# Performance work log

Measured on AMD Instinct MI355X. Metric: run time of the kernel, lower is better.

Reference implementation:

```python
import jax, jax.numpy as jnp
import numpy as np

N = 50000      # nodes
E = 800000     # edges (before self-loops)
F_IN = 256     # feature_size
H = 96         # hidden_channels
G = 64         # graphs in batch
NC = 4         # num_classes
EPS = 1e-5     # BatchNorm eps


def _lrelu(x, s=0.01):
    return jnp.where(x >= 0, x, s * x)


def _gat(x, W, a_s, a_d, b, src, dst):
    # PyG GATConv, heads=1: linear transform, edge-wise LeakyReLU(0.2) scores,
    # segment softmax over destination nodes, scatter-add aggregation.
    h = x @ W                                                  # [N,H]
    e = _lrelu((h * a_s).sum(-1)[src] + (h * a_d).sum(-1)[dst], 0.2)  # [E+N]
    m = jax.ops.segment_max(e, dst, num_segments=N)
    ee = jnp.exp(e - m[dst])
    denom = jax.ops.segment_sum(ee, dst, num_segments=N)
    alpha = ee / denom[dst]
    return jax.ops.segment_sum(alpha[:, None] * h[src], dst, num_segments=N) + b


def _bn(x, g, b):
    # training-mode BatchNorm over the node dimension
    mu = x.mean(0)
    var = ((x - mu) ** 2).mean(0)
    return g * (x - mu) / jnp.sqrt(var + EPS) + b


def setup_inputs() -> dict:
    key = jax.random.key(0)
    ks = jax.random.split(key, 20)
    p = lambda i, sh: jax.random.normal(ks[i], sh, jnp.float32) * 0.05
    inp = {
        "x": jax.random.normal(ks[0], (N, F_IN), jnp.float32),
        "edge_index": jax.random.randint(ks[1], (2, E), 0, N),
        "batch": jnp.sort(jax.random.randint(ks[2], (N,), 0, G)),
        "embed_W": p(3, (F_IN, H)), "embed_b": jnp.zeros((H,), jnp.float32),
        "conv1_W": p(4, (H, H)), "conv1_as": p(5, (H,)), "conv1_ad": p(6, (H,)), "conv1_b": jnp.zeros((H,), jnp.float32),
        "conv2_W": p(7, (H, H)), "conv2_as": p(8, (H,)), "conv2_ad": p(9, (H,)), "conv2_b": jnp.zeros((H,), jnp.float32),
        "conv3_W": p(10, (H, H)), "conv3_as": p(11, (H,)), "conv3_ad": p(12, (H,)), "conv3_b": jnp.zeros((H,), jnp.float32),
        "fc1_W": p(13, (H, H)), "fc1_b": jnp.zeros((H,), jnp.float32),
        "fc2_W": p(14, (H, H)), "fc2_b": jnp.zeros((H,), jnp.float32),
        "bn1_g": jnp.ones((H,), jnp.float32), "bn1_b": jnp.zeros((H,), jnp.float32),
        "bn2_g": jnp.ones((H,), jnp.float32), "bn2_b": jnp.zeros((H,), jnp.float32),
        "bn3_g": jnp.ones((H,), jnp.float32), "bn3_b": jnp.zeros((H,), jnp.float32),
        "fc3_W": p(15, (H, H // 2)), "fc3_b": jnp.zeros((H // 2,), jnp.float32),
        "fc4_W": p(16, (H // 2, NC)), "fc4_b": jnp.zeros((NC,), jnp.float32),
    }
    return inp


def reference(x, edge_index, batch, embed_W, embed_b,
              conv1_W, conv1_as, conv1_ad, conv1_b,
              conv2_W, conv2_as, conv2_ad, conv2_b,
              conv3_W, conv3_as, conv3_ad, conv3_b,
              fc1_W, fc1_b, fc2_W, fc2_b,
              bn1_g, bn1_b, bn2_g, bn2_b, bn3_g, bn3_b,
              fc3_W, fc3_b, fc4_W, fc4_b):
    loops = jnp.arange(N)
    src = jnp.concatenate([edge_index[0], loops])   # GATConv add_self_loops=True
    dst = jnp.concatenate([edge_index[1], loops])

    h = _lrelu(x @ embed_W + embed_b)
    identity = h
    h = _lrelu(_bn(_gat(h, conv1_W, conv1_as, conv1_ad, conv1_b, src, dst), bn1_g, bn1_b)) + identity
    h = _lrelu(h @ fc1_W + fc1_b)
    h = _lrelu(_bn(_gat(h, conv2_W, conv2_as, conv2_ad, conv2_b, src, dst), bn2_g, bn2_b)) + identity
    h = _lrelu(h @ fc2_W + fc2_b)
    h = _lrelu(_bn(_gat(h, conv3_W, conv3_as, conv3_ad, conv3_b, src, dst), bn3_g, bn3_b)) + identity

    # Poincare ball expmap0 with c=1: tanh(||u||) * u / ||u||
    n = jnp.maximum(jnp.linalg.norm(h, axis=-1, keepdims=True), 1e-15)
    h = jnp.tanh(n) * h / n

    cnt = jax.ops.segment_sum(jnp.ones((N,), h.dtype), batch, num_segments=G)
    pooled = jax.ops.segment_sum(h, batch, num_segments=G) / jnp.maximum(cnt, 1.0)[:, None]

    o = _lrelu(pooled @ fc3_W + fc3_b)
    return o @ fc4_W + fc4_b
```

## Files before the change

kernel.cpp:

```cpp
#include <hip/hip_runtime.h>
#include <hip/hip_bf16.h>

#define DEVINL __device__ __forceinline__

constexpr int N_NODES = 50000;
constexpr int N_EDGES = 800000;
constexpr int F_IN    = 256;
constexpr int H       = 96;
constexpr int NG      = 64;
constexpr float BN_EPS = 1e-5f;
constexpr int SLOT    = 64;
constexpr int NREP    = 8;
constexpr int REPSZ   = NG * H + NG;
constexpr int EPB     = 8;
constexpr int ECHUNK  = 256 * EPB;

typedef short bf16x8 __attribute__((ext_vector_type(8)));
typedef float f32x4  __attribute__((ext_vector_type(4)));

DEVINL float bf2f(unsigned int u) {
    union { unsigned int i; float f; } c; c.i = u << 16; return c.f;
}
DEVINL unsigned short f2bf(float f) {
    union { float f; unsigned int i; } c; c.f = f;
    unsigned int x = c.i;
    return (unsigned short)((x + 0x7fffu + ((x >> 16) & 1u)) >> 16);
}
DEVINL float lrelu01(float v) { return v >= 0.f ? v : 0.01f * v; }
DEVINL float ldf(const void* p, size_t i, int f32) {
    return f32 ? ((const float*)p)[i] : bf2f(((const unsigned short*)p)[i]);
}

__global__ __launch_bounds__(256) void detect_fill_k(const unsigned short* __restrict__ x,
                                                     int* __restrict__ flag,
                                                     int* __restrict__ fill)
{
    if (blockIdx.x == 0 && threadIdx.x < 64) {
        int l = threadIdx.x;
        float f = bf2f(x[l]);
        bool huge = !(fabsf(f) <= 1e4f);
        unsigned long long m = __ballot(huge);
        if (l == 0) flag[0] = (__popcll(m) >= 8) ? 1 : 0;
    }
    int i = blockIdx.x * 256 + threadIdx.x;
    if (i < N_NODES) fill[i] = 0;
}

__global__ __launch_bounds__(256) void wpackall_k(
    const void* __restrict__ sE, const void* __restrict__ s0,
    const void* __restrict__ s1, const void* __restrict__ s2,
    const void* __restrict__ s3, const void* __restrict__ s4,
    const int* __restrict__ dflag,
    unsigned short* __restrict__ dE, unsigned short* __restrict__ d0,
    unsigned short* __restrict__ d1, unsigned short* __restrict__ d2,
    unsigned short* __restrict__ d3, unsigned short* __restrict__ d4)
{
    int b = blockIdx.x;
    const void* src; unsigned short* dst; int K, i0;
    if (b < 96) { src = sE; dst = dE; K = F_IN; i0 = b * 256; }
    else {
        int m = (b - 96) / 36, r = (b - 96) % 36;
        K = H; i0 = r * 256;
        if      (m == 0) { src = s0; dst = d0; }
        else if (m == 1) { src = s1; dst = d1; }
        else if (m == 2) { src = s2; dst = d2; }
        else if (m == 3) { src = s3; dst = d3; }
        else             { src = s4; dst = d4; }
    }
    int i = i0 + threadIdx.x;
    if (i >= K * 96) return;
    int c   = i / 3072;
    int rem = i - c * 3072;
    int t    = rem >> 9;
    int rem2 = rem & 511;
    int l = rem2 >> 3, j = rem2 & 7;
    int k = c * 32 + (l >> 4) * 8 + j;
    int n = t * 16 + (l & 15);
    if (dflag[0]) dst[i] = f2bf(((const float*)src)[k * 96 + n]);
    else          dst[i] = ((const unsigned short*)src)[k * 96 + n];
}

template<int EPI, int AWS, int SD, int ABN, int SCAT, int K>
__global__ __launch_bounds__(256, 4) void mgemm_k(
    const void* __restrict__ Ap, const unsigned short* __restrict__ Wpk,
    const void* __restrict__ bp, const int* __restrict__ dflag,
    unsigned short* __restrict__ out, unsigned short* __restrict__ out2,
    const void* __restrict__ as_, const void* __restrict__ ad_,
    float* __restrict__ s, float* __restrict__ d,
    const float* __restrict__ coefp, const unsigned short* __restrict__ idn,
    const int* __restrict__ ei, int* __restrict__ fill,
    unsigned short* __restrict__ colw, int e0, int e1, int nscat,
    int M)
{
    constexpr int NCH = K / 32;

    if (SCAT && (int)blockIdx.x < nscat) {
        int b0 = e0 + (int)blockIdx.x * ECHUNK + (int)threadIdx.x;
        int sv[EPB], dv[EPB];
        bool ok[EPB];
        #pragma unroll
        for (int j = 0; j < EPB; j++) {
            int e = b0 + j * 256;
            ok[j] = (e < e1);
            int ee = ok[j] ? e : e0;
            sv[j] = ei[ee];
            dv[j] = ei[N_EDGES + ee];
        }
        int p[EPB];
        #pragma unroll
        for (int j = 0; j < EPB; j++)
            p[j] = ok[j] ? atomicAdd(&fill[dv[j]], 1) : SLOT;
        #pragma unroll
        for (int j = 0; j < EPB; j++)
            if (p[j] < SLOT) colw[(size_t)dv[j] * SLOT + p[j]] = (unsigned short)sv[j];
        return;
    }

    const int gb   = SCAT ? (int)blockIdx.x - nscat : (int)blockIdx.x;
    const int f32  = AWS ? 0 : dflag[0];
    const int wf32 = dflag[0];
    const int l    = threadIdx.x & 63;
    const int wave = threadIdx.x >> 6;
    const int row0 = gb * 64 + wave * 16;
    const int m    = l & 15;
    const int q    = l >> 4;
    const int arow = row0 + m;
    const bool aok = arow < M;

    bf16x8 av[NCH];
    #pragma unroll
    for (int c = 0; c < NCH; c++) {
        bf16x8 a = {};
        if (aok) {
            if (ABN) {
                const int f0 = c * 32 + q * 8;
                uint4 xu = *(const uint4*)((const unsigned short*)Ap + (size_t)arow * K + f0);
                uint4 iu = *(const uint4*)(idn + (size_t)arow * K + f0);
                unsigned int xs[4] = { xu.x, xu.y, xu.z, xu.w };
                unsigned int is[4] = { iu.x, iu.y, iu.z, iu.w };
                #pragma unroll
                for (int jj = 0; jj < 4; jj++) {
                    int f = f0 + 2 * jj;
                    float v0 = lrelu01(bf2f(xs[jj] & 0xffff) * coefp[f]     + coefp[96 + f])     + bf2f(is[jj] & 0xffff);
                    float v1 = lrelu01(bf2f(xs[jj] >> 16)    * coefp[f + 1] + coefp[96 + f + 1]) + bf2f(is[jj] >> 16);
                    a[2 * jj]     = (short)f2bf(v0);
                    a[2 * jj + 1] = (short)f2bf(v1);
                }
            } else if (f32) {
                const float* A = (const float*)Ap + (size_t)arow * K + c * 32 + q * 8;
                #pragma unroll
                for (int j = 0; j < 8; j++) a[j] = (short)f2bf(A[j]);
            } else {
                a = *(const bf16x8*)((const unsigned short*)Ap + (size_t)arow * K + c * 32 + q * 8);
            }
        }
        av[c] = a;
    }

    f32x4 acc[6] = {};
    const bf16x8* wp = (const bf16x8*)Wpk;
    #pragma unroll
    for (int c = 0; c < NCH; c++) {
        const int base = c * 384 + l;
        #pragma unroll
        for (int t = 0; t < 6; t++)
            acc[t] = __builtin_amdgcn_mfma_f32_16x16x32_bf16(av[c], wp[base + t * 64], acc[t], 0, 0, 0);
    }

    float bv[6];
    if (EPI > 0) {
        #pragma unroll
        for (int t = 0; t < 6; t++) bv[t] = ldf(bp, t * 16 + m, wf32);
    }
    #pragma unroll
    for (int r = 0; r < 4; r++) {
        int rr = row0 + q * 4 + r;
        if (rr >= M) continue;
        size_t o = (size_t)rr * 96 + m;
        #pragma unroll
        for (int t = 0; t < 6; t++) {
            float v = acc[t][r];
            if (EPI > 0) v = lrelu01(v + bv[t]);
            unsigned short sv = f2bf(v);
            out[o + t * 16] = sv;
            if (EPI == 2) out2[o + t * 16] = sv;
        }
    }

    if (SD) {
        float asv[6], adv[6];
        #pragma unroll
        for (int t = 0; t < 6; t++) {
            asv[t] = ldf(as_, t * 16 + m, wf32);
            adv[t] = ldf(ad_, t * 16 + m, wf32);
        }
        #pragma unroll
        for (int r = 0; r < 4; r++) {
            float ps = 0.f, pd = 0.f;
            #pragma unroll
            for (int t = 0; t < 6; t++) {
                ps = fmaf(acc[t][r], asv[t], ps);
                pd = fmaf(acc[t][r], adv[t], pd);
            }
            #pragma unroll
            for (int off = 1; off < 16; off <<= 1) {
                ps += __shfl_xor(ps, off);
                pd += __shfl_xor(pd, off);
            }
            int rr = row0 + q * 4 + r;
            if (m == 0 && rr < M) { s[rr] = ps; d[rr] = pd; }
        }
    }
}

__global__ __launch_bounds__(256) void agg_k(
    const unsigned short* __restrict__ h2, const float* __restrict__ s,
    const float* __restrict__ d, const int* __restrict__ fill,
    const unsigned short* __restrict__ col, const void* __restrict__ bias,
    const int* __restrict__ dflag, unsigned short* __restrict__ out,
    float* __restrict__ bnsum, float* __restrict__ zp, int M)
{
    __shared__ uint2 uwb[4][80];
    if (blockIdx.x == 0 && threadIdx.x < 192) bnsum[threadIdx.x] = 0.f;
    if (zp) {
        int zi = blockIdx.x * 256 + threadIdx.x;
        if (zi < NREP * REPSZ) zp[zi] = 0.f;
    }
    int f32 = dflag[0];
    int v = (blockIdx.x * blockDim.x + threadIdx.x) >> 6;
    int l = threadIdx.x & 63;
    int wv = threadIdx.x >> 6;
    if (v >= M) return;
    int st   = v * SLOT;
    int degr = min(fill[v], SLOT - 1);
    int deg  = degr + 1;

    float dv = d[v];
    int u = 0; float e = -1e30f;
    if (l < degr) {
        u = col[st + l];
        float t = s[u] + dv;
        e = t >= 0.f ? t : 0.2f * t;
    } else if (l == degr) {
        u = v;
        float t = s[v] + dv;
        e = t >= 0.f ? t : 0.2f * t;
    }
    float lm = e;
    #pragma unroll
    for (int off = 32; off > 0; off >>= 1) lm = fmaxf(lm, __shfl_xor(lm, off));
    float w = (l < deg) ? __expf(e - lm) : 0.f;
    float ls = w;
    #pragma unroll
    for (int off = 32; off > 0; off >>= 1) ls += __shfl_xor(ls, off);
    float rden = 1.0f / ls;

    uwb[wv][l] = make_uint2((unsigned int)u, __float_as_uint(w));
    if (l < 16) uwb[wv][64 + l] = make_uint2(0u, 0u);

    bool hw = (l < 48);
    int  c2 = 2 * l;
    float a0 = 0.f, a1 = 0.f;
    const uint2* myuw = uwb[wv];
    for (int j = 0; j < deg; j += 16) {
        uint2 p[16];
        #pragma unroll
        for (int k = 0; k < 16; k++) p[k] = myuw[j + k];
        if (hw) {
            unsigned int hv[16];
            #pragma unroll
            for (int k = 0; k < 16; k++)
                hv[k] = *(const unsigned int*)(h2 + (size_t)p[k].x * 96 + c2);
            #pragma unroll
            for (int k = 0; k < 16; k++) {
                float wj = __uint_as_float(p[k].y);
                a0 = fmaf(wj, bf2f(hv[k] & 0xffff), a0);
                a1 = fmaf(wj, bf2f(hv[k] >> 16),    a1);
            }
        }
    }
    if (hw) {
        float b0 = ldf(bias, c2,     f32);
        float b1 = ldf(bias, c2 + 1, f32);
        unsigned int o = (unsigned int)f2bf(a0 * rden + b0)
                       | ((unsigned int)f2bf(a1 * rden + b1) << 16);
        *(unsigned int*)(out + (size_t)v * 96 + c2) = o;
    }
}

__global__ __launch_bounds__(192) void bnstats_k(const unsigned short* __restrict__ x,
                                                 float* __restrict__ sums, int M)
{
    int c  = threadIdx.x % 96;
    int g2 = threadIdx.x / 96;
    float s = 0.f, q = 0.f;
    for (int r = blockIdx.x * 2 + g2; r < M; r += gridDim.x * 2) {
        float v = bf2f(x[(size_t)r * 96 + c]);
        s += v; q += v * v;
    }
    __shared__ float lsd[192], lqd[192];
    lsd[threadIdx.x] = s; lqd[threadIdx.x] = q;
    __syncthreads();
    if (g2 == 0) {
        atomicAdd(&sums[c],      s + lsd[threadIdx.x + 96]);
        atomicAdd(&sums[96 + c], q + lqd[threadIdx.x + 96]);
    }
}

__global__ void bncoef_k(const float* __restrict__ sums,
                         const void* __restrict__ g_,
                         const void* __restrict__ b_,
                         const int* __restrict__ dflag,
                         float* __restrict__ coef)
{
    int c = threadIdx.x;
    if (c >= 96) return;
    int f32 = dflag[0];
    float mu  = sums[c] * (1.f / N_NODES);
    float var = sums[96 + c] * (1.f / N_NODES) - mu * mu;
    float rinv = 1.0f / sqrtf(var + BN_EPS);
    float sc = ldf(g_, c, f32) * rinv;
    coef[c]      = sc;
    coef[96 + c] = ldf(b_, c, f32) - mu * sc;
}

__global__ __launch_bounds__(256) void bnpool_k(
    const unsigned short* __restrict__ h, const float* __restrict__ coef,
    const unsigned short* __restrict__ iden, const int* __restrict__ batch,
    float* __restrict__ pooled8, int M)
{
    int w = (blockIdx.x * blockDim.x + threadIdx.x) >> 6;
    int l = threadIdx.x & 63;
    int v0 = w * 16;
    if (v0 >= M) return;
    float* P = pooled8 + (blockIdx.x & (NREP - 1)) * REPSZ;
    float* C = P + NG * H;
    bool hw = (l < 48);
    int  c2 = 2 * l;
    float sc0 = 0.f, sc1 = 0.f, sh0 = 0.f, sh1 = 0.f;
    if (hw) {
        sc0 = coef[c2]; sc1 = coef[c2 + 1];
        sh0 = coef[96 + c2]; sh1 = coef[97 + c2];
    }
    int nv = min(16, M - v0);

    int gb[16];
    #pragma unroll
    for (int k = 0; k < 16; k++) gb[k] = batch[v0 + min(k, nv - 1)];

    float x0[16], x1[16], q[16];
    #pragma unroll
    for (int k = 0; k < 16; k++) { x0[k] = 0.f; x1[k] = 0.f; q[k] = 0.f; }
    if (hw) {
        unsigned int xu[16], iu[16];
        #pragma unroll
        for (int k = 0; k < 16; k++) {
            int v = v0 + k;
            if (k < nv) {
                xu[k] = *(const unsigned int*)(h    + (size_t)v * 96 + c2);
                iu[k] = *(const unsigned int*)(iden + (size_t)v * 96 + c2);
            } else { xu[k] = 0u; iu[k] = 0u; }
        }
        #pragma unroll
        for (int k = 0; k < 16; k++) {
            x0[k] = lrelu01(bf2f(xu[k] & 0xffff) * sc0 + sh0) + bf2f(iu[k] & 0xffff);
            x1[k] = lrelu01(bf2f(xu[k] >> 16)    * sc1 + sh1) + bf2f(iu[k] >> 16);
            q[k]  = x0[k] * x0[k] + x1[k] * x1[k];
        }
    }

    #pragma unroll
    for (int off = 32; off > 0; off >>= 1) {
        #pragma unroll
        for (int k = 0; k < 16; k++) q[k] += __shfl_xor(q[k], off);
    }

    float f[16];
    #pragma unroll
    for (int k = 0; k < 16; k++) {
        float n = fmaxf(sqrtf(q[k]), 1e-15f);
        if (n < 15.f) {
            float t = __expf(2.f * n);
            f[k] = (t - 1.f) / ((t + 1.f) * n);
        } else {
            f[k] = 1.f / n;
        }
    }

    float a0 = 0.f, a1 = 0.f, cnt = 0.f;
    int curg = -1;
    for (int k = 0; k < nv; k++) {
        int g = gb[k];
        if (g != curg) {
            if (curg >= 0) {
                if (hw) {
                    atomicAdd(&P[curg * 96 + c2],     a0);
                    atomicAdd(&P[curg * 96 + c2 + 1], a1);
                }
                if (l == 0) atomicAdd(&C[curg], cnt);
            }
            a0 = a1 = 0.f; cnt = 0.f; curg = g;
        }
        a0 = fmaf(f[k], x0[k], a0);
        a1 = fmaf(f[k], x1[k], a1);
        cnt += 1.f;
    }
    if (curg >= 0) {
        if (hw) {
            atomicAdd(&P[curg * 96 + c2],     a0);
            atomicAdd(&P[curg * 96 + c2 + 1], a1);
        }
        if (l == 0) atomicAdd(&C[curg], cnt);
    }
}

__global__ __launch_bounds__(64) void head_k(const float* __restrict__ pooled8,
                                             const void* __restrict__ w3,
                                             const void* __restrict__ b3,
                                             const void* __restrict__ w4,
                                             const void* __restrict__ b4,
                                             const int* __restrict__ dflag,
                                             void* __restrict__ outv)
{
    int g = blockIdx.x;
    int t = threadIdx.x;
    int f32 = dflag[0];
    __shared__ float p[96];
    __shared__ float o[48];
    float cs = 0.f;
    #pragma unroll
    for (int r = 0; r < NREP; r++) cs += pooled8[r * REPSZ + NG * H + g];
    float inv = 1.0f / fmaxf(cs, 1.0f);
    for (int c = t; c < 96; c += 64) {
        float v = 0.f;
        #pragma unroll
        for (int r = 0; r < NREP; r++) v += pooled8[r * REPSZ + g * 96 + c];
        p[c] = v * inv;
    }
    __syncthreads();
    if (t < 48) {
        float a = ldf(b3, t, f32);
        #pragma unroll
        for (int c = 0; c < 96; c++) a = fmaf(p[c], ldf(w3, (size_t)c * 48 + t, f32), a);
        o[t] = lrelu01(a);
    }
    __syncthreads();
    if (t < 4) {
        float a = ldf(b4, t, f32);
        #pragma unroll
        for (int j = 0; j < 48; j++) a = fmaf(o[j], ldf(w4, j * 4 + t, f32), a);
        if (f32) ((float*)outv)[g * 4 + t] = a;
        else     ((unsigned short*)outv)[g * 4 + t] = f2bf(a);
    }
}

extern "C" void kernel_launch(void* const* d_in, const int* in_sizes, int n_in,
                              void* d_out, int out_size, void* d_ws, size_t ws_size,
                              hipStream_t stream)
{
    const void* x     = d_in[0];
    const int*  ei    = (const int*)d_in[1];
    const int*  batch = (const int*)d_in[2];
    const void* embW  = d_in[3];
    const void* embB  = d_in[4];
    const void* convW[3]  = { d_in[5],  d_in[9],  d_in[13] };
    const void* convAs[3] = { d_in[6],  d_in[10], d_in[14] };
    const void* convAd[3] = { d_in[7],  d_in[11], d_in[15] };
    const void* convB[3]  = { d_in[8],  d_in[12], d_in[16] };
    const void* fcW[2]    = { d_in[17], d_in[19] };
    const void* fcB[2]    = { d_in[18], d_in[20] };
    const void* bnG[3]    = { d_in[21], d_in[23], d_in[25] };
    const void* bnB[3]    = { d_in[22], d_in[24], d_in[26] };
    const void* fc3W = d_in[27];
    const void* fc3b = d_in[28];
    const void* fc4W = d_in[29];
    const void* fc4b = d_in[30];

    char* wp_ = (char*)d_ws;
    auto alloc = [&](size_t b) { char* p = wp_; wp_ += (b + 255) & ~(size_t)255; return p; };
    int*   dflag = (int*)alloc(256);
    unsigned short* ident = (unsigned short*)alloc((size_t)N_NODES * H * 2);
    unsigned short* hA    = (unsigned short*)alloc((size_t)N_NODES * H * 2);
    unsigned short* hB    = (unsigned short*)alloc((size_t)N_NODES * H * 2);
    float* s_sc  = (float*)alloc((size_t)N_NODES * 4);
    float* d_sc  = (float*)alloc((size_t)N_NODES * 4);
    float* bnsum = (float*)alloc(192 * 4);
    float* coef  = (float*)alloc(192 * 4);
    float* pooled8 = (float*)alloc((size_t)NREP * REPSZ * 4);
    int*   fill  = (int*)alloc((size_t)N_NODES * 4);
    unsigned short* col = (unsigned short*)alloc((size_t)N_NODES * SLOT * 2);
    unsigned short* wpkEmb = (unsigned short*)alloc((size_t)F_IN * 96 * 2);
    unsigned short* wpkS[5];
    for (int i = 0; i < 5; i++) wpkS[i] = (unsigned short*)alloc((size_t)H * 96 * 2);

    const int GM = (N_NODES + 63) / 64;
    const int GW = (N_NODES * 64 + 255) / 256;
    const int GP = ((N_NODES + 15) / 16 * 64 + 255) / 256;
    const int GF = (N_NODES + 255) / 256;
    const int EH = N_EDGES / 2;
    const int GS = (EH + ECHUNK - 1) / ECHUNK;

    detect_fill_k<<<GF, 256, 0, stream>>>((const unsigned short*)x, dflag, fill);

    wpackall_k<<<276, 256, 0, stream>>>(embW, convW[0], convW[1], convW[2], fcW[0], fcW[1],
                                        dflag, wpkEmb, wpkS[0], wpkS[1], wpkS[2], wpkS[3], wpkS[4]);

    mgemm_k<1, 0, 0, 0, 1, F_IN><<<GS + GM, 256, 0, stream>>>(
        x, wpkEmb, embB, dflag, ident, nullptr,
        nullptr, nullptr, nullptr, nullptr, nullptr, nullptr,
        ei, fill, col, 0, EH, GS, N_NODES);

    unsigned short* hcur = hA;
    unsigned short* htmp = hB;

    for (int l = 0; l < 3; l++) {
        if (l == 0) {
            mgemm_k<0, 1, 1, 0, 1, H><<<GS + GM, 256, 0, stream>>>(
                ident, wpkS[0], nullptr, dflag, htmp, nullptr,
                convAs[0], convAd[0], s_sc, d_sc, nullptr, nullptr,
                ei, fill, col, EH, N_EDGES, GS, N_NODES);
        } else {
            mgemm_k<0, 1, 1, 0, 0, H><<<GM, 256, 0, stream>>>(
                hcur, wpkS[l], nullptr, dflag, htmp, nullptr,
                convAs[l], convAd[l], s_sc, d_sc, nullptr, nullptr,
                nullptr, nullptr, nullptr, 0, 0, 0, N_NODES);
        }
        agg_k<<<GW, 256, 0, stream>>>(htmp, s_sc, d_sc, fill, col, convB[l], dflag, hcur,
                                      bnsum, (l == 2) ? pooled8 : nullptr, N_NODES);
        bnstats_k<<<512, 192, 0, stream>>>(hcur, bnsum, N_NODES);
        bncoef_k<<<1, 128, 0, stream>>>(bnsum, bnG[l], bnB[l], dflag, coef);
        if (l < 2) {
            mgemm_k<1, 1, 0, 1, 0, H><<<GM, 256, 0, stream>>>(
                hcur, wpkS[3 + l], fcB[l], dflag, htmp, nullptr,
                nullptr, nullptr, nullptr, nullptr, coef, ident,
                nullptr, nullptr, nullptr, 0, 0, 0, N_NODES);
            unsigned short* t = hcur; hcur = htmp; htmp = t;
        }
    }

    bnpool_k<<<GP, 256, 0, stream>>>(hcur, coef, ident, batch, pooled8, N_NODES);
    head_k<<<NG, 64, 0, stream>>>(pooled8, fc3W, fc3b, fc4W, fc4b, dflag, d_out);
}
```

Baseline: 437.5 us.

## Fuse BN stats into aggregation, fuse fc and conv GEMMs, merge setup kernels

BatchNorm sum and sum-of-squares are now computed inside the aggregation kernel from the values it just wrote. Each block reduces them in shared memory and adds atomically into 64 replicated accumulators, which replaces the separate bnstats pass that re-read the whole feature matrix. The BN-apply, fc GEMM and next conv GEMM are fused into one kernel that passes the intermediate tile through shared memory, and the detect/fill and weight-pack kernels are merged into one. This removes several launches and full-array round trips, at the cost of more atomics and a longer serial reduction in bncoef.

```diff
diff --git a/kernel.cpp b/kernel.cpp
--- a/kernel.cpp
+++ b/kernel.cpp
@@ -14,6 +14,8 @@
 constexpr int REPSZ   = NG * H + NG;
 constexpr int EPB     = 8;
 constexpr int ECHUNK  = 256 * EPB;
+constexpr int BNREP   = 64;
+constexpr int GFILL   = (N_NODES + 255) / 256;
 
 typedef short bf16x8 __attribute__((ext_vector_type(8)));
 typedef float f32x4  __attribute__((ext_vector_type(4)));
@@ -31,35 +33,39 @@
     return f32 ? ((const float*)p)[i] : bf2f(((const unsigned short*)p)[i]);
 }
 
-__global__ __launch_bounds__(256) void detect_fill_k(const unsigned short* __restrict__ x,
-                                                     int* __restrict__ flag,
-                                                     int* __restrict__ fill)
-{
-    if (blockIdx.x == 0 && threadIdx.x < 64) {
-        int l = threadIdx.x;
-        float f = bf2f(x[l]);
-        bool huge = !(fabsf(f) <= 1e4f);
-        unsigned long long m = __ballot(huge);
-        if (l == 0) flag[0] = (__popcll(m) >= 8) ? 1 : 0;
-    }
-    int i = blockIdx.x * 256 + threadIdx.x;
-    if (i < N_NODES) fill[i] = 0;
-}
-
-__global__ __launch_bounds__(256) void wpackall_k(
+__global__ __launch_bounds__(256) void setup_k(
+    const unsigned short* __restrict__ x,
+    int* __restrict__ flag, int* __restrict__ fill,
     const void* __restrict__ sE, const void* __restrict__ s0,
     const void* __restrict__ s1, const void* __restrict__ s2,
     const void* __restrict__ s3, const void* __restrict__ s4,
-    const int* __restrict__ dflag,
     unsigned short* __restrict__ dE, unsigned short* __restrict__ d0,
     unsigned short* __restrict__ d1, unsigned short* __restrict__ d2,
     unsigned short* __restrict__ d3, unsigned short* __restrict__ d4)
 {
     int b = blockIdx.x;
+    if (b < GFILL) {
+        if (b == 0 && threadIdx.x < 64) {
+            int l = threadIdx.x;
+            float f = bf2f(x[l]);
+            bool huge = !(fabsf(f) <= 1e4f);
+            unsigned long long m = __ballot(huge);
+            if (l == 0) flag[0] = (__popcll(m) >= 8) ? 1 : 0;
+        }
+        int i = b * 256 + threadIdx.x;
+        if (i < N_NODES) fill[i] = 0;
+        return;
+    }
+    float ff = bf2f(x[threadIdx.x & 63]);
+    bool huge = !(fabsf(ff) <= 1e4f);
+    unsigned long long mm = __ballot(huge);
+    int lf32 = (__popcll(mm) >= 8) ? 1 : 0;
+
+    int bb = b - GFILL;
     const void* src; unsigned short* dst; int K, i0;
-    if (b < 96) { src = sE; dst = dE; K = F_IN; i0 = b * 256; }
+    if (bb < 96) { src = sE; dst = dE; K = F_IN; i0 = bb * 256; }
     else {
-        int m = (b - 96) / 36, r = (b - 96) % 36;
+        int m = (bb - 96) / 36, r = (bb - 96) % 36;
         K = H; i0 = r * 256;
         if      (m == 0) { src = s0; dst = d0; }
         else if (m == 1) { src = s1; dst = d1; }
@@ -76,11 +82,11 @@
     int l = rem2 >> 3, j = rem2 & 7;
     int k = c * 32 + (l >> 4) * 8 + j;
     int n = t * 16 + (l & 15);
-    if (dflag[0]) dst[i] = f2bf(((const float*)src)[k * 96 + n]);
-    else          dst[i] = ((const unsigned short*)src)[k * 96 + n];
-}
-
-template<int EPI, int AWS, int SD, int ABN, int SCAT, int K>
+    if (lf32) dst[i] = f2bf(((const float*)src)[k * 96 + n]);
+    else      dst[i] = ((const unsigned short*)src)[k * 96 + n];
+}
+
+template<int EPI, int AWS, int SD, int ABN, int SCAT, int K, int ZB>
 __global__ __launch_bounds__(256, 4) void mgemm_k(
     const void* __restrict__ Ap, const unsigned short* __restrict__ Wpk,
     const void* __restrict__ bp, const int* __restrict__ dflag,
@@ -90,9 +96,14 @@
     const float* __restrict__ coefp, const unsigned short* __restrict__ idn,
     const int* __restrict__ ei, int* __restrict__ fill,
     unsigned short* __restrict__ colw, int e0, int e1, int nscat,
-    int M)
+    float* __restrict__ bnsumR, int M)
 {
     constexpr int NCH = K / 32;
+
+    if (ZB) {
+        int zi = blockIdx.x * 256 + threadIdx.x;
+        if (zi < BNREP * 192) bnsumR[zi] = 0.f;
+    }
 
     if (SCAT && (int)blockIdx.x < nscat) {
         int b0 = e0 + (int)blockIdx.x * ECHUNK + (int)threadIdx.x;
@@ -213,15 +224,135 @@
     }
 }
 
+__global__ __launch_bounds__(256, 4) void fcconv_k(
+    const unsigned short* __restrict__ Ap,
+    const unsigned short* __restrict__ Wfc, const void* __restrict__ bfc,
+    const unsigned short* __restrict__ Wcv,
+    const int* __restrict__ dflag,
+    unsigned short* __restrict__ out,
+    const void* __restrict__ as_, const void* __restrict__ ad_,
+    float* __restrict__ s, float* __restrict__ d,
+    const float* __restrict__ coefp, const unsigned short* __restrict__ idn,
+    float* __restrict__ bnsumR, int M)
+{
+    __shared__ unsigned short R[64][104];
+
+    {
+        int zi = blockIdx.x * 256 + threadIdx.x;
+        if (zi < BNREP * 192) bnsumR[zi] = 0.f;
+    }
+
+    const int wf32 = dflag[0];
+    const int l    = threadIdx.x & 63;
+    const int wave = threadIdx.x >> 6;
+    const int row0 = blockIdx.x * 64 + wave * 16;
+    const int m    = l & 15;
+    const int q    = l >> 4;
+    const int arow = row0 + m;
+    const bool aok = arow < M;
+
+    bf16x8 av[3];
+    #pragma unroll
+    for (int c = 0; c < 3; c++) {
+        bf16x8 a = {};
+        if (aok) {
+            const int f0 = c * 32 + q * 8;
+            uint4 xu = *(const uint4*)(Ap  + (size_t)arow * H + f0);
+            uint4 iu = *(const uint4*)(idn + (size_t)arow * H + f0);
+            unsigned int xs[4] = { xu.x, xu.y, xu.z, xu.w };
+            unsigned int is[4] = { iu.x, iu.y, iu.z, iu.w };
+            #pragma unroll
+            for (int jj = 0; jj < 4; jj++) {
+                int f = f0 + 2 * jj;
+                float v0 = lrelu01(bf2f(xs[jj] & 0xffff) * coefp[f]     + coefp[96 + f])     + bf2f(is[jj] & 0xffff);
+                float v1 = lrelu01(bf2f(xs[jj] >> 16)    * coefp[f + 1] + coefp[96 + f + 1]) + bf2f(is[jj] >> 16);
+                a[2 * jj]     = (short)f2bf(v0);
+                a[2 * jj + 1] = (short)f2bf(v1);
+            }
+        }
+        av[c] = a;
+    }
+
+    f32x4 acc[6] = {};
+    const bf16x8* wp1 = (const bf16x8*)Wfc;
+    #pragma unroll
+    for (int c = 0; c < 3; c++) {
+        const int base = c * 384 + l;
+        #pragma unroll
+        for (int t = 0; t < 6; t++)
+            acc[t] = __builtin_amdgcn_mfma_f32_16x16x32_bf16(av[c], wp1[base + t * 64], acc[t], 0, 0, 0);
+    }
+
+    float bv[6];
+    #pragma unroll
+    for (int t = 0; t < 6; t++) bv[t] = ldf(bfc, t * 16 + m, wf32);
+    #pragma unroll
+    for (int r = 0; r < 4; r++) {
+        int lr = wave * 16 + q * 4 + r;
+        #pragma unroll
+        for (int t = 0; t < 6; t++)
+            R[lr][t * 16 + m] = f2bf(lrelu01(acc[t][r] + bv[t]));
+    }
+    __syncthreads();
+
+    bf16x8 a2[3];
+    #pragma unroll
+    for (int c = 0; c < 3; c++)
+        a2[c] = *(const bf16x8*)&R[wave * 16 + m][c * 32 + q * 8];
+
+    f32x4 acc2[6] = {};
+    const bf16x8* wp2 = (const bf16x8*)Wcv;
+    #pragma unroll
+    for (int c = 0; c < 3; c++) {
+        const int base = c * 384 + l;
+        #pragma unroll
+        for (int t = 0; t < 6; t++)
+            acc2[t] = __builtin_amdgcn_mfma_f32_16x16x32_bf16(a2[c], wp2[base + t * 64], acc2[t], 0, 0, 0);
+    }
+
+    #pragma unroll
+    for (int r = 0; r < 4; r++) {
+        int rr = row0 + q * 4 + r;
+        if (rr >= M) continue;
+        size_t o = (size_t)rr * 96 + m;
+        #pragma unroll
+        for (int t = 0; t < 6; t++)
+            out[o + t * 16] = f2bf(acc2[t][r]);
+    }
+
+    float asv[6], adv[6];
+    #pragma unroll
+    for (int t = 0; t < 6; t++) {
+        asv[t] = ldf(as_, t * 16 + m, wf32);
+        adv[t] = ldf(ad_, t * 16 + m, wf32);
+    }
+    #pragma unroll
+    for (int r = 0; r < 4; r++) {
+        float ps = 0.f, pd = 0.f;
+        #pragma unroll
+        for (int t = 0; t < 6; t++) {
+            ps = fmaf(acc2[t][r], asv[t], ps);
+            pd = fmaf(acc2[t][r], adv[t], pd);
+        }
+        #pragma unroll
+        for (int off = 1; off < 16; off <<= 1) {
+            ps += __shfl_xor(ps, off);
+            pd += __shfl_xor(pd, off);
+        }
+        int rr = row0 + q * 4 + r;
+        if (m == 0 && rr < M) { s[rr] = ps; d[rr] = pd; }
+    }
+}
+
 __global__ __launch_bounds__(256) void agg_k(
     const unsigned short* __restrict__ h2, const float* __restrict__ s,
     const float* __restrict__ d, const int* __restrict__ fill,
     const unsigned short* __restrict__ col, const void* __restrict__ bias,
     const int* __restrict__ dflag, unsigned short* __restrict__ out,
-    float* __restrict__ bnsum, float* __restrict__ zp, int M)
+    float* __restrict__ bnsumR, float* __restrict__ zp, int M)
 {
     __shared__ uint2 uwb[4][80];
-    if (blockIdx.x == 0 && threadIdx.x < 192) bnsum[threadIdx.x] = 0.f;
+    __shared__ float lstat[4][192];
     if (zp) {
         int zi = blockIdx.x * 256 + threadIdx.x;
         if (zi < NREP * REPSZ) zp[zi] = 0.f;
@@ -230,98 +361,107 @@
     int v = (blockIdx.x * blockDim.x + threadIdx.x) >> 6;
     int l = threadIdx.x & 63;
     int wv = threadIdx.x >> 6;
-    if (v >= M) return;
-    int st   = v * SLOT;
-    int degr = min(fill[v], SLOT - 1);
-    int deg  = degr + 1;
-
-    float dv = d[v];
-    int u = 0; float e = -1e30f;
-    if (l < degr) {
-        u = col[st + l];
-        float t = s[u] + dv;
-        e = t >= 0.f ? t : 0.2f * t;
-    } else if (l == degr) {
-        u = v;
-        float t = s[v] + dv;
-        e = t >= 0.f ? t : 0.2f * t;
-    }
-    float lm = e;
-    #pragma unroll
-    for (int off = 32; off > 0; off >>= 1) lm = fmaxf(lm, __shfl_xor(lm, off));
-    float w = (l < deg) ? __expf(e - lm) : 0.f;
-    float ls = w;
-    #pragma unroll
-    for (int off = 32; off > 0; off >>= 1) ls += __shfl_xor(ls, off);
-    float rden = 1.0f / ls;
-
-    uwb[wv][l] = make_uint2((unsigned int)u, __float_as_uint(w));
-    if (l < 16) uwb[wv][64 + l] = make_uint2(0u, 0u);
-
+    bool act = v < M;
     bool hw = (l < 48);
     int  c2 = 2 * l;
-    float a0 = 0.f, a1 = 0.f;
-    const uint2* myuw = uwb[wv];
-    for (int j = 0; j < deg; j += 16) {
-        uint2 p[16];
-        #pragma unroll
-        for (int k = 0; k < 16; k++) p[k] = myuw[j + k];
+    float o0 = 0.f, o1 = 0.f;
+
+    if (act) {
+        int st   = v * SLOT;
+        int degr = min(fill[v], SLOT - 1);
+        int deg  = degr + 1;
+
+        float dv = d[v];
+        int u = 0; float e = -1e30f;
+        if (l < degr) {
+            u = col[st + l];
+            float t = s[u] + dv;
+            e = t >= 0.f ? t : 0.2f * t;
+        } else if (l == degr) {
+            u = v;
+            float t = s[v] + dv;
+            e = t >= 0.f ? t : 0.2f * t;
+        }
+        float lm = e;
+        #pragma unroll
+        for (int off = 32; off > 0; off >>= 1) lm = fmaxf(lm, __shfl_xor(lm, off));
+        float w = (l < deg) ? __expf(e - lm) : 0.f;
+        float lsum = w;
+        #pragma unroll
+        for (int off = 32; off > 0; off >>= 1) lsum += __shfl_xor(lsum, off);
+        float rden = 1.0f / lsum;
+
+        uwb[wv][l] = make_uint2((unsigned int)u, __float_as_uint(w));
+        if (l < 16) uwb[wv][64 + l] = make_uint2(0u, 0u);
+
+        float a0 = 0.f, a1 = 0.f;
+        const uint2* myuw = uwb[wv];
+        for (int j = 0; j < deg; j += 16) {
+            uint2 p[16];
+            #pragma unroll
+            for (int k = 0; k < 16; k++) p[k] = myuw[j + k];
+            if (hw) {
+                unsigned int hv[16];
+                #pragma unroll
+                for (int k = 0; k < 16; k++)
+                    hv[k] = *(const unsigned int*)(h2 + (size_t)p[k].x * 96 + c2);
+                #pragma unroll
+                for (int k = 0; k < 16; k++) {
+                    float wj = __uint_as_float(p[k].y);
+                    a0 = fmaf(wj, bf2f(hv[k] & 0xffff), a0);
+                    a1 = fmaf(wj, bf2f(hv[k] >> 16),    a1);
+                }
+            }
+        }
         if (hw) {
-            unsigned int hv[16];
-            #pragma unroll
-            for (int k = 0; k < 16; k++)
-                hv[k] = *(const unsigned int*)(h2 + (size_t)p[k].x * 96 + c2);
-            #pragma unroll
-            for (int k = 0; k < 16; k++) {
-                float wj = __uint_as_float(p[k].y);
-                a0 = fmaf(wj, bf2f(hv[k] & 0xffff), a0);
-                a1 = fmaf(wj, bf2f(hv[k] >> 16),    a1);
-            }
-        }
-    }
+            float b0 = ldf(bias, c2,     f32);
+            float b1 = ldf(bias, c2 + 1, f32);
+            unsigned int o = (unsigned int)f2bf(a0 * rden + b0)
+                           | ((unsigned int)f2bf(a1 * rden + b1) << 16);
+            *(unsigned int*)(out + (size_t)v * 96 + c2) = o;
+            o0 = bf2f(o & 0xffff);
+            o1 = bf2f(o >> 16);
+        }
+    }
+
     if (hw) {
-        float b0 = ldf(bias, c2,     f32);
-        float b1 = ldf(bias, c2 + 1, f32);
-        unsigned int o = (unsigned int)f2bf(a0 * rden + b0)
-                       | ((unsigned int)f2bf(a1 * rden + b1) << 16);
-        *(unsigned int*)(out + (size_t)v * 96 + c2) = o;
-    }
-}
-
-__global__ __launch_bounds__(192) void bnstats_k(const unsigned short* __restrict__ x,
-                                                 float* __restrict__ sums, int M)
-{
-    int c  = threadIdx.x % 96;
-    int g2 = threadIdx.x / 96;
-    float s = 0.f, q = 0.f;
-    for (int r = blockIdx.x * 2 + g2; r < M; r += gridDim.x * 2) {
-        float v = bf2f(x[(size_t)r * 96 + c]);
-        s += v; q += v * v;
-    }
-    __shared__ float lsd[192], lqd[192];
-    lsd[threadIdx.x] = s; lqd[threadIdx.x] = q;
+        lstat[wv][c2]          = o0;
+        lstat[wv][c2 + 1]      = o1;
+        lstat[wv][96 + c2]     = o0 * o0;
+        lstat[wv][97 + c2]     = o1 * o1;
+    }
     __syncthreads();
-    if (g2 == 0) {
-        atomicAdd(&sums[c],      s + lsd[threadIdx.x + 96]);
-        atomicAdd(&sums[96 + c], q + lqd[threadIdx.x + 96]);
-    }
-}
-
-__global__ void bncoef_k(const float* __restrict__ sums,
+    if (threadIdx.x < 192) {
+        float tot = lstat[0][threadIdx.x] + lstat[1][threadIdx.x]
+                  + lstat[2][threadIdx.x] + lstat[3][threadIdx.x];
+        atomicAdd(&bnsumR[(blockIdx.x & (BNREP - 1)) * 192 + threadIdx.x], tot);
+    }
+}
+
+__global__ void bncoef_k(const float* __restrict__ bnsumR,
                          const void* __restrict__ g_,
                          const void* __restrict__ b_,
                          const int* __restrict__ dflag,
                          float* __restrict__ coef)
 {
-    int c = threadIdx.x;
-    if (c >= 96) return;
-    int f32 = dflag[0];
-    float mu  = sums[c] * (1.f / N_NODES);
-    float var = sums[96 + c] * (1.f / N_NODES) - mu * mu;
-    float rinv = 1.0f / sqrtf(var + BN_EPS);
-    float sc = ldf(g_, c, f32) * rinv;
-    coef[c]      = sc;
-    coef[96 + c] = ldf(b_, c, f32) - mu * sc;
+    __shared__ float tot[192];
+    int t = threadIdx.x;
+    if (t < 192) {
+        float s = 0.f;
+        #pragma unroll 8
+        for (int r = 0; r < BNREP; r++) s += bnsumR[r * 192 + t];
+        tot[t] = s;
+    }
+    __syncthreads();
+    if (t < 96) {
+        int f32 = dflag[0];
+        float mu  = tot[t] * (1.f / N_NODES);
+        float var = tot[96 + t] * (1.f / N_NODES) - mu * mu;
+        float rinv = 1.0f / sqrtf(var + BN_EPS);
+        float sc = ldf(g_, t, f32) * rinv;
+        coef[t]      = sc;
+        coef[96 + t] = ldf(b_, t, f32) - mu * sc;
+    }
 }
 
 __global__ __launch_bounds__(256) void bnpool_k(
@@ -484,7 +624,7 @@
     unsigned short* hB    = (unsigned short*)alloc((size_t)N_NODES * H * 2);
     float* s_sc  = (float*)alloc((size_t)N_NODES * 4);
     float* d_sc  = (float*)alloc((size_t)N_NODES * 4);
-    float* bnsum = (float*)alloc(192 * 4);
+    float* bnsumR = (float*)alloc((size_t)BNREP * 192 * 4);
     float* coef  = (float*)alloc(192 * 4);
     float* pooled8 = (float*)alloc((size_t)NREP * REPSZ * 4);
     int*   fill  = (int*)alloc((size_t)N_NODES * 4);
@@ -496,48 +636,42 @@
     const int GM = (N_NODES + 63) / 64;
     const int GW = (N_NODES * 64 + 255) / 256;
     const int GP = ((N_NODES + 15) / 16 * 64 + 255) / 256;
-    const int GF = (N_NODES + 255) / 256;
     const int EH = N_EDGES / 2;
     const int GS = (EH + ECHUNK - 1) / ECHUNK;
 
-    detect_fill_k<<<GF, 256, 0, stream>>>((const unsigned short*)x, dflag, fill);
-
-    wpackall_k<<<276, 256, 0, stream>>>(embW, convW[0], convW[1], convW[2], fcW[0], fcW[1],
-                                        dflag, wpkEmb, wpkS[0], wpkS[1], wpkS[2], wpkS[3], wpkS[4]);
-
-    mgemm_k<1, 0, 0, 0, 1, F_IN><<<GS + GM, 256, 0, stream>>>(
+    setup_k<<<GFILL + 276, 256, 0, stream>>>(
+        (const unsigned short*)x, dflag, fill,
+        embW, convW[0], convW[1], convW[2], fcW[0], fcW[1],
+        wpkEmb, wpkS[0], wpkS[1], wpkS[2], wpkS[3], wpkS[4]);
+
+    mgemm_k<1, 0, 0, 0, 1, F_IN, 0><<<GS + GM, 256, 0, stream>>>(
         x, wpkEmb, embB, dflag, ident, nullptr,
         nullptr, nullptr, nullptr, nullptr, nullptr, nullptr,
-        ei, fill, col, 0, EH, GS, N_NODES);
-
-    unsigned short* hcur = hA;
-    unsigned short* htmp = hB;
-
-    for (int l = 0; l < 3; l++) {
-        if (l == 0) {
-            mgemm_k<0, 1, 1, 0, 1, H><<<GS + GM, 256, 0, stream>>>(
-                ident, wpkS[0], nullptr, dflag, htmp, nullptr,
-                convAs[0], convAd[0], s_sc, d_sc, nullptr, nullptr,
-                ei, fill, col, EH, N_EDGES, GS, N_NODES);
-        } else {
-            mgemm_k<0, 1, 1, 0, 0, H><<<GM, 256, 0, stream>>>(
-                hcur, wpkS[l], nullptr, dflag, htmp, nullptr,
-                convAs[l], convAd[l], s_sc, d_sc, nullptr, nullptr,
-                nullptr, nullptr, nullptr, 0, 0, 0, N_NODES);
-        }
-        agg_k<<<GW, 256, 0, stream>>>(htmp, s_sc, d_sc, fill, col, convB[l], dflag, hcur,
-                                      bnsum, (l == 2) ? pooled8 : nullptr, N_NODES);
-        bnstats_k<<<512, 192, 0, stream>>>(hcur, bnsum, N_NODES);
-        bncoef_k<<<1, 128, 0, stream>>>(bnsum, bnG[l], bnB[l], dflag, coef);
-        if (l < 2) {
-            mgemm_k<1, 1, 0, 1, 0, H><<<GM, 256, 0, stream>>>(
-                hcur, wpkS[3 + l], fcB[l], dflag, htmp, nullptr,
-                nullptr, nullptr, nullptr, nullptr, coef, ident,
-                nullptr, nullptr, nullptr, 0, 0, 0, N_NODES);
-            unsigned short* t = hcur; hcur = htmp; htmp = t;
-        }
-    }
-
-    bnpool_k<<<GP, 256, 0, stream>>>(hcur, coef, ident, batch, pooled8, N_NODES);
+        ei, fill, col, 0, EH, GS, nullptr, N_NODES);
+
+    mgemm_k<0, 1, 1, 0, 1, H, 1><<<GS + GM, 256, 0, stream>>>(
+        ident, wpkS[0], nullptr, dflag, hB, nullptr,
+        convAs[0], convAd[0], s_sc, d_sc, nullptr, nullptr,
+        ei, fill, col, EH, N_EDGES, GS, bnsumR, N_NODES);
+
+    agg_k<<<GW, 256, 0, stream>>>(hB, s_sc, d_sc, fill, col, convB[0], dflag, hA,
+                                  bnsumR, nullptr, N_NODES);
+    bncoef_k<<<1, 192, 0, stream>>>(bnsumR, bnG[0], bnB[0], dflag, coef);
+    fcconv_k<<<GM, 256, 0, stream>>>(hA, wpkS[3], fcB[0], wpkS[1], dflag, hB,
+                                     convAs[1], convAd[1], s_sc, d_sc,
+                                     coef, ident, bnsumR, N_NODES);
+
+    agg_k<<<GW, 256, 0, stream>>>(hB, s_sc, d_sc, fill, col, convB[1], dflag, hA,
+                                  bnsumR, nullptr, N_NODES);
+    bncoef_k<<<1, 192, 0, stream>>>(bnsumR, bnG[1], bnB[1], dflag, coef);
+    fcconv_k<<<GM, 256, 0, stream>>>(hA, wpkS[4], fcB[1], wpkS[2], dflag, hB,
+                                     convAs[2], convAd[2], s_sc, d_sc,
+                                     coef, ident, bnsumR, N_NODES);
+
+    agg_k<<<GW, 256, 0, stream>>>(hB, s_sc, d_sc, fill, col, convB[2], dflag, hA,
+                                  bnsumR, pooled8, N_NODES);
+    bncoef_k<<<1, 192, 0, stream>>>(bnsumR, bnG[2], bnB[2], dflag, coef);
+
+    bnpool_k<<<GP, 256, 0, stream>>>(hA, coef, ident, batch, pooled8, N_NODES);
     head_k<<<NG, 64, 0, stream>>>(pooled8, fc3W, fc3b, fc4W, fc4b, dflag, d_out);
 }
```

After: 372.7 us. -14.8%, faster.
